# Kernel tuning notes

Hardware: AMD Instinct MI355X
Metric: run time of the kernel (lower is better)

Reference implementation:

```python
import jax, jax.numpy as jnp
import numpy as np

B = 8192
L = 2  # number of clipped photonic layers


def _pauli_z_matrix():
    # Z expectation per wire for each of the 16 basis states; wire 0 = MSB.
    k = np.arange(16)
    Z = np.stack([1 - 2 * ((k >> 3) & 1),
                  1 - 2 * ((k >> 2) & 1),
                  1 - 2 * ((k >> 1) & 1),
                  1 - 2 * (k & 1)], axis=1).astype(np.float32)
    return jnp.asarray(Z)  # (16, 4)


def setup_inputs() -> dict:
    key = jax.random.key(0)
    ks = jax.random.split(key, 14)
    x = jax.random.normal(ks[0], (B, 1, 28, 28), dtype=jnp.float32)
    # input photonic layer (no clip)
    w_in = 0.5 * jax.random.normal(ks[1], (2, 2), dtype=jnp.float32)
    b_in = 0.1 * jax.random.normal(ks[2], (2,), dtype=jnp.float32)
    scale_in = 1.0 + 0.1 * jax.random.normal(ks[3], (2,), dtype=jnp.float32)
    shift_in = 0.05 * jax.random.normal(ks[4], (2,), dtype=jnp.float32)
    # L clipped photonic layers (clip applied at construction in torch)
    Wc = jnp.clip(0.5 * jax.random.normal(ks[5], (L, 2, 2), dtype=jnp.float32), -5.0, 5.0)
    bc = jnp.clip(0.1 * jax.random.normal(ks[6], (L, 2), dtype=jnp.float32), -5.0, 5.0)
    scalec = 1.0 + 0.1 * jax.random.normal(ks[7], (L, 2), dtype=jnp.float32)
    shiftc = 0.05 * jax.random.normal(ks[8], (L, 2), dtype=jnp.float32)
    # final linear of classical branch: Linear(2, 1)
    w_out = 0.5 * jax.random.normal(ks[9], (1, 2), dtype=jnp.float32)
    b_out = 0.1 * jax.random.normal(ks[10], (1,), dtype=jnp.float32)
    # fixed random 16x16 unitary standing in for tq.RandomLayer(n_ops=8, 4 wires)
    rng = np.random.default_rng(0)
    A = rng.normal(size=(16, 16)) + 1j * rng.normal(size=(16, 16))
    Q, _ = np.linalg.qr(A)
    U_re = jnp.asarray(Q.real.astype(np.float32))
    U_im = jnp.asarray(Q.imag.astype(np.float32))
    # classifier Linear(785, 1)  (original declares 786 but combined feat is 785)
    w_cls = 0.03 * jax.random.normal(ks[11], (1, 785), dtype=jnp.float32)
    b_cls = 0.1 * jax.random.normal(ks[12], (1,), dtype=jnp.float32)
    return {"x": x, "w_in": w_in, "b_in": b_in, "scale_in": scale_in,
            "shift_in": shift_in, "Wc": Wc, "bc": bc, "scalec": scalec,
            "shiftc": shiftc, "w_out": w_out, "b_out": b_out,
            "U_re": U_re, "U_im": U_im, "w_cls": w_cls, "b_cls": b_cls}


def reference(x, w_in, b_in, scale_in, shift_in, Wc, bc, scalec, shiftc,
              w_out, b_out, U_re, U_im, w_cls, b_cls):
    bsz = x.shape[0]
    # ---- classical branch: mean/std features through photonic-style MLP ----
    mean = jnp.mean(x, axis=(1, 2, 3))[:, None]
    std = jnp.std(x, axis=(1, 2, 3), ddof=1)[:, None]  # torch unbiased std
    h = jnp.concatenate([mean, std], axis=1)  # (B, 2)
    h = jnp.tanh(h @ w_in.T + b_in) * scale_in + shift_in
    for i in range(Wc.shape[0]):
        h = jnp.tanh(h @ Wc[i].T + bc[i]) * scalec[i] + shiftc[i]
    cls_out = h @ w_out.T + b_out  # (B, 1)
    # ---- quantum branch: all 196 2x2 patches batched in one pass ----
    img = x.reshape(bsz, 28, 28)
    # (B,14,2,14,2) -> (B,14,14,2,2) -> (B,196,4) with patch pixel order
    # [x[r,c], x[r,c+1], x[r+1,c], x[r+1,c+1]] matching the torch loop.
    p = img.reshape(bsz, 14, 2, 14, 2).transpose(0, 1, 3, 2, 4).reshape(bsz, 196, 4)
    half = 0.5 * p
    a = jnp.stack([jnp.cos(half), jnp.sin(half)], axis=-1)  # (B,196,4,2) RY|0> amps
    # product state over 4 qubits -> (B,196,16)
    psi = jnp.einsum('bpi,bpj,bpk,bpl->bpijkl',
                     a[:, :, 0], a[:, :, 1], a[:, :, 2], a[:, :, 3]
                     ).reshape(bsz, 196, 16)
    re = psi @ U_re.T
    im = psi @ U_im.T
    probs = re * re + im * im  # (B,196,16)
    Z = _pauli_z_matrix()
    qfeat = (probs @ Z).reshape(bsz, 196 * 4)  # (B, 784)
    # ---- fuse + classify ----
    combined = jnp.concatenate([cls_out, qfeat], axis=1)  # (B, 785)
    logits = combined @ w_cls.T + b_cls
    return jax.nn.sigmoid(logits)
```

## Files before the change

### kernel.cpp

```cpp
#include <hip/hip_runtime.h>
#include <math.h>


#define NPIX 784
#define NPATCH 196

__global__ __launch_bounds__(256) void fraud_kernel(
    const float* __restrict__ x,
    const float* __restrict__ w_in,
    const float* __restrict__ b_in,
    const float* __restrict__ scale_in,
    const float* __restrict__ shift_in,
    const float* __restrict__ Wc,
    const float* __restrict__ bc,
    const float* __restrict__ scalec,
    const float* __restrict__ shiftc,
    const float* __restrict__ w_out,
    const float* __restrict__ b_out,
    const float* __restrict__ U_re,
    const float* __restrict__ U_im,
    const float* __restrict__ w_cls,
    const float* __restrict__ b_cls,
    float* __restrict__ out)
{
    const int img  = blockIdx.x;
    const int tid  = threadIdx.x;
    const int lane = tid & 63;
    const int wave = tid >> 6;

    const float* xp = x + (size_t)img * NPIX;

    float sum = 0.f, sumsq = 0.f, qsum = 0.f;

    if (tid < NPATCH) {
        const int r = tid / 14;
        const int c = tid - r * 14;
        const float2 top = *(const float2*)(xp + (2 * r) * 28 + 2 * c);
        const float2 bot = *(const float2*)(xp + (2 * r + 1) * 28 + 2 * c);
        const float x0 = top.x, x1 = top.y, x2 = bot.x, x3 = bot.y;

        sum   = x0 + x1 + x2 + x3;
        sumsq = x0 * x0 + x1 * x1 + x2 * x2 + x3 * x3;

        const float c0 = __cosf(0.5f * x0), s0 = __sinf(0.5f * x0);
        const float c1 = __cosf(0.5f * x1), s1 = __sinf(0.5f * x1);
        const float c2 = __cosf(0.5f * x2), s2 = __sinf(0.5f * x2);
        const float c3 = __cosf(0.5f * x3), s3 = __sinf(0.5f * x3);

        float p01[4] = { c0 * c1, c0 * s1, s0 * c1, s0 * s1 };
        float p23[4] = { c2 * c3, c2 * s3, s2 * c3, s2 * s3 };
        float psi[16];
        #pragma unroll
        for (int h = 0; h < 4; ++h) {
            #pragma unroll
            for (int l = 0; l < 4; ++l) {
                psi[h * 4 + l] = p01[h] * p23[l];
            }
        }

        const float wq0 = w_cls[1 + tid * 4 + 0];
        const float wq1 = w_cls[1 + tid * 4 + 1];
        const float wq2 = w_cls[1 + tid * 4 + 2];
        const float wq3 = w_cls[1 + tid * 4 + 3];
        float hi[4] = { wq0 + wq1, wq0 - wq1, -wq0 + wq1, -wq0 - wq1 };
        float lo[4] = { wq2 + wq3, wq2 - wq3, -wq2 + wq3, -wq2 - wq3 };

        #pragma unroll
        for (int k = 0; k < 16; ++k) {
            const float* ur = U_re + k * 16;
            const float* ui = U_im + k * 16;
            float re = 0.f, im = 0.f;
            #pragma unroll
            for (int m = 0; m < 16; ++m) {
                re = fmaf(ur[m], psi[m], re);
                im = fmaf(ui[m], psi[m], im);
            }
            const float prob = re * re + im * im;
            qsum = fmaf(prob, hi[k >> 2] + lo[k & 3], qsum);
        }
    }

    #pragma unroll
    for (int off = 32; off > 0; off >>= 1) {
        sum   += __shfl_down(sum,   off, 64);
        sumsq += __shfl_down(sumsq, off, 64);
        qsum  += __shfl_down(qsum,  off, 64);
    }

    __shared__ float red[3][4];
    if (lane == 0) {
        red[0][wave] = sum;
        red[1][wave] = sumsq;
        red[2][wave] = qsum;
    }
    __syncthreads();

    if (tid == 0) {
        const float S  = red[0][0] + red[0][1] + red[0][2] + red[0][3];
        const float SS = red[1][0] + red[1][1] + red[1][2] + red[1][3];
        const float QS = red[2][0] + red[2][1] + red[2][2] + red[2][3];

        const float mean = S * (1.f / 784.f);
        float var = (SS - S * S * (1.f / 784.f)) * (1.f / 783.f);
        var = fmaxf(var, 0.f);
        const float stdv = sqrtf(var);

        float h0 = mean, h1 = stdv;
        {
            const float t0 = tanhf(h0 * w_in[0] + h1 * w_in[1] + b_in[0]);
            const float t1 = tanhf(h0 * w_in[2] + h1 * w_in[3] + b_in[1]);
            h0 = t0 * scale_in[0] + shift_in[0];
            h1 = t1 * scale_in[1] + shift_in[1];
        }
        #pragma unroll
        for (int i = 0; i < 2; ++i) {
            const float t0 = tanhf(h0 * Wc[i * 4 + 0] + h1 * Wc[i * 4 + 1] + bc[i * 2 + 0]);
            const float t1 = tanhf(h0 * Wc[i * 4 + 2] + h1 * Wc[i * 4 + 3] + bc[i * 2 + 1]);
            h0 = t0 * scalec[i * 2 + 0] + shiftc[i * 2 + 0];
            h1 = t1 * scalec[i * 2 + 1] + shiftc[i * 2 + 1];
        }
        const float cls   = h0 * w_out[0] + h1 * w_out[1] + b_out[0];
        const float logit = b_cls[0] + w_cls[0] * cls + QS;
        out[img] = 1.f / (1.f + __expf(-logit));
    }
}

extern "C" void kernel_launch(void* const* d_in, const int* in_sizes, int n_in,
                              void* d_out, int out_size, void* d_ws, size_t ws_size,
                              hipStream_t stream) {
    const float* x        = (const float*)d_in[0];
    const float* w_in     = (const float*)d_in[1];
    const float* b_in     = (const float*)d_in[2];
    const float* scale_in = (const float*)d_in[3];
    const float* shift_in = (const float*)d_in[4];
    const float* Wc       = (const float*)d_in[5];
    const float* bc       = (const float*)d_in[6];
    const float* scalec   = (const float*)d_in[7];
    const float* shiftc   = (const float*)d_in[8];
    const float* w_out    = (const float*)d_in[9];
    const float* b_out    = (const float*)d_in[10];
    const float* U_re     = (const float*)d_in[11];
    const float* U_im     = (const float*)d_in[12];
    const float* w_cls    = (const float*)d_in[13];
    const float* b_cls    = (const float*)d_in[14];
    float* out = (float*)d_out;

    const int B = out_size;
    fraud_kernel<<<B, 256, 0, stream>>>(x, w_in, b_in, scale_in, shift_in,
                                        Wc, bc, scalec, shiftc, w_out, b_out,
                                        U_re, U_im, w_cls, b_cls, out);
}
```

Baseline: 119.4 us.

## Flatten patch work across batch with wave-split atomic reduction and finalize kernel

Replaces the one-block-per-image kernel (which left 60 of 256 threads idle) with a flat grid over all image patches. Each wave reduces its partial sums separately for up to two images and atomically adds them into a workspace. A second small kernel then computes the per-image statistics, the classical branch and the sigmoid. This adds a memset, an extra kernel launch and global atomics in exchange for full lane utilisation.

```diff
diff --git a/kernel.cpp b/kernel.cpp
--- a/kernel.cpp
+++ b/kernel.cpp
@@ -2,11 +2,99 @@
 #include <math.h>
 
 
-#define NPIX 784
 #define NPATCH 196
+#define NIMG   8192
+#define NTOTAL (NIMG * NPATCH)
 
-__global__ __launch_bounds__(256) void fraud_kernel(
+__global__ __launch_bounds__(256) void patch_kernel(
     const float* __restrict__ x,
+    const float* __restrict__ U_re,
+    const float* __restrict__ U_im,
+    const float* __restrict__ w_cls,
+    float* __restrict__ accS,
+    float* __restrict__ accSS,
+    float* __restrict__ accQ)
+{
+    const int g    = blockIdx.x * 256 + threadIdx.x;
+    const int img  = g / NPATCH;
+    const int p    = g - img * NPATCH;
+    const int r    = p / 14;
+    const int c    = p - r * 14;
+    const int lane = threadIdx.x & 63;
+
+    const float* xp = x + (size_t)img * 784;
+    const float2 top = *(const float2*)(xp + (2 * r) * 28 + 2 * c);
+    const float2 bot = *(const float2*)(xp + (2 * r + 1) * 28 + 2 * c);
+    const float x0 = top.x, x1 = top.y, x2 = bot.x, x3 = bot.y;
+
+    float sum   = x0 + x1 + x2 + x3;
+    float sumsq = x0 * x0 + x1 * x1 + x2 * x2 + x3 * x3;
+
+    const float c0 = __cosf(0.5f * x0), s0 = __sinf(0.5f * x0);
+    const float c1 = __cosf(0.5f * x1), s1 = __sinf(0.5f * x1);
+    const float c2 = __cosf(0.5f * x2), s2 = __sinf(0.5f * x2);
+    const float c3 = __cosf(0.5f * x3), s3 = __sinf(0.5f * x3);
+
+    float p01[4] = { c0 * c1, c0 * s1, s0 * c1, s0 * s1 };
+    float p23[4] = { c2 * c3, c2 * s3, s2 * c3, s2 * s3 };
+    float psi[16];
+    #pragma unroll
+    for (int h = 0; h < 4; ++h)
+        #pragma unroll
+        for (int l = 0; l < 4; ++l)
+            psi[h * 4 + l] = p01[h] * p23[l];
+
+    const float wq0 = w_cls[1 + p * 4 + 0];
+    const float wq1 = w_cls[1 + p * 4 + 1];
+    const float wq2 = w_cls[1 + p * 4 + 2];
+    const float wq3 = w_cls[1 + p * 4 + 3];
+    float hi[4] = { wq0 + wq1, wq0 - wq1, -wq0 + wq1, -wq0 - wq1 };
+    float lo[4] = { wq2 + wq3, wq2 - wq3, -wq2 + wq3, -wq2 - wq3 };
+
+    float qsum = 0.f;
+    #pragma unroll
+    for (int k = 0; k < 16; ++k) {
+        const float* ur = U_re + k * 16;
+        const float* ui = U_im + k * 16;
+        float re = 0.f, im = 0.f;
+        #pragma unroll
+        for (int m = 0; m < 16; ++m) {
+            re = fmaf(ur[m], psi[m], re);
+            im = fmaf(ui[m], psi[m], im);
+        }
+        const float prob = re * re + im * im;
+        qsum = fmaf(prob, hi[k >> 2] + lo[k & 3], qsum);
+    }
+
+    const int imgF = __builtin_amdgcn_readfirstlane(img);
+    const bool first = (img == imgF);
+    float aS = first ? sum   : 0.f;  float bS = sum   - aS;
+    float aV = first ? sumsq : 0.f;  float bV = sumsq - aV;
+    float aQ = first ? qsum  : 0.f;  float bQ = qsum  - aQ;
+
+    #pragma unroll
+    for (int off = 1; off < 64; off <<= 1) {
+        aS += __shfl_xor(aS, off, 64);  bS += __shfl_xor(bS, off, 64);
+        aV += __shfl_xor(aV, off, 64);  bV += __shfl_xor(bV, off, 64);
+        aQ += __shfl_xor(aQ, off, 64);  bQ += __shfl_xor(bQ, off, 64);
+    }
+
+    if (lane == 0) {
+        atomicAdd(accS  + imgF, aS);
+        atomicAdd(accSS + imgF, aV);
+        atomicAdd(accQ  + imgF, aQ);
+    }
+    if (lane == 63 && img != imgF) {
+        atomicAdd(accS  + img, bS);
+        atomicAdd(accSS + img, bV);
+        atomicAdd(accQ  + img, bQ);
+    }
+}
+
+__global__ __launch_bounds__(256) void final_kernel(
+    const float* __restrict__ accS,
+    const float* __restrict__ accSS,
+    const float* __restrict__ accQ,
     const float* __restrict__ w_in,
     const float* __restrict__ b_in,
     const float* __restrict__ scale_in,
@@ -17,112 +105,37 @@
     const float* __restrict__ shiftc,
     const float* __restrict__ w_out,
     const float* __restrict__ b_out,
-    const float* __restrict__ U_re,
-    const float* __restrict__ U_im,
     const float* __restrict__ w_cls,
     const float* __restrict__ b_cls,
     float* __restrict__ out)
 {
-    const int img  = blockIdx.x;
-    const int tid  = threadIdx.x;
-    const int lane = tid & 63;
-    const int wave = tid >> 6;
+    const int i = blockIdx.x * 256 + threadIdx.x;
+    const float S  = accS[i];
+    const float SS = accSS[i];
+    const float QS = accQ[i];
 
-    const float* xp = x + (size_t)img * NPIX;
+    const float mean = S * (1.f / 784.f);
+    float var = (SS - S * S * (1.f / 784.f)) * (1.f / 783.f);
+    var = fmaxf(var, 0.f);
+    const float stdv = sqrtf(var);
 
-    float sum = 0.f, sumsq = 0.f, qsum = 0.f;
-
-    if (tid < NPATCH) {
-        const int r = tid / 14;
-        const int c = tid - r * 14;
-        const float2 top = *(const float2*)(xp + (2 * r) * 28 + 2 * c);
-        const float2 bot = *(const float2*)(xp + (2 * r + 1) * 28 + 2 * c);
-        const float x0 = top.x, x1 = top.y, x2 = bot.x, x3 = bot.y;
-
-        sum   = x0 + x1 + x2 + x3;
-        sumsq = x0 * x0 + x1 * x1 + x2 * x2 + x3 * x3;
-
-        const float c0 = __cosf(0.5f * x0), s0 = __sinf(0.5f * x0);
-        const float c1 = __cosf(0.5f * x1), s1 = __sinf(0.5f * x1);
-        const float c2 = __cosf(0.5f * x2), s2 = __sinf(0.5f * x2);
-        const float c3 = __cosf(0.5f * x3), s3 = __sinf(0.5f * x3);
-
-        float p01[4] = { c0 * c1, c0 * s1, s0 * c1, s0 * s1 };
-        float p23[4] = { c2 * c3, c2 * s3, s2 * c3, s2 * s3 };
-        float psi[16];
-        #pragma unroll
-        for (int h = 0; h < 4; ++h) {
-            #pragma unroll
-            for (int l = 0; l < 4; ++l) {
-                psi[h * 4 + l] = p01[h] * p23[l];
-            }
-        }
-
-        const float wq0 = w_cls[1 + tid * 4 + 0];
-        const float wq1 = w_cls[1 + tid * 4 + 1];
-        const float wq2 = w_cls[1 + tid * 4 + 2];
-        const float wq3 = w_cls[1 + tid * 4 + 3];
-        float hi[4] = { wq0 + wq1, wq0 - wq1, -wq0 + wq1, -wq0 - wq1 };
-        float lo[4] = { wq2 + wq3, wq2 - wq3, -wq2 + wq3, -wq2 - wq3 };
-
-        #pragma unroll
-        for (int k = 0; k < 16; ++k) {
-            const float* ur = U_re + k * 16;
-            const float* ui = U_im + k * 16;
-            float re = 0.f, im = 0.f;
-            #pragma unroll
-            for (int m = 0; m < 16; ++m) {
-                re = fmaf(ur[m], psi[m], re);
-                im = fmaf(ui[m], psi[m], im);
-            }
-            const float prob = re * re + im * im;
-            qsum = fmaf(prob, hi[k >> 2] + lo[k & 3], qsum);
-        }
+    float h0 = mean, h1 = stdv;
+    {
+        const float t0 = tanhf(h0 * w_in[0] + h1 * w_in[1] + b_in[0]);
+        const float t1 = tanhf(h0 * w_in[2] + h1 * w_in[3] + b_in[1]);
+        h0 = t0 * scale_in[0] + shift_in[0];
+        h1 = t1 * scale_in[1] + shift_in[1];
     }
-
     #pragma unroll
-    for (int off = 32; off > 0; off >>= 1) {
-        sum   += __shfl_down(sum,   off, 64);
-        sumsq += __shfl_down(sumsq, off, 64);
-        qsum  += __shfl_down(qsum,  off, 64);
+    for (int l = 0; l < 2; ++l) {
+        const float t0 = tanhf(h0 * Wc[l * 4 + 0] + h1 * Wc[l * 4 + 1] + bc[l * 2 + 0]);
+        const float t1 = tanhf(h0 * Wc[l * 4 + 2] + h1 * Wc[l * 4 + 3] + bc[l * 2 + 1]);
+        h0 = t0 * scalec[l * 2 + 0] + shiftc[l * 2 + 0];
+        h1 = t1 * scalec[l * 2 + 1] + shiftc[l * 2 + 1];
     }
-
-    __shared__ float red[3][4];
-    if (lane == 0) {
-        red[0][wave] = sum;
-        red[1][wave] = sumsq;
-        red[2][wave] = qsum;
-    }
-    __syncthreads();
-
-    if (tid == 0) {
-        const float S  = red[0][0] + red[0][1] + red[0][2] + red[0][3];
-        const float SS = red[1][0] + red[1][1] + red[1][2] + red[1][3];
-        const float QS = red[2][0] + red[2][1] + red[2][2] + red[2][3];
-
-        const float mean = S * (1.f / 784.f);
-        float var = (SS - S * S * (1.f / 784.f)) * (1.f / 783.f);
-        var = fmaxf(var, 0.f);
-        const float stdv = sqrtf(var);
-
-        float h0 = mean, h1 = stdv;
-        {
-            const float t0 = tanhf(h0 * w_in[0] + h1 * w_in[1] + b_in[0]);
-            const float t1 = tanhf(h0 * w_in[2] + h1 * w_in[3] + b_in[1]);
-            h0 = t0 * scale_in[0] + shift_in[0];
-            h1 = t1 * scale_in[1] + shift_in[1];
-        }
-        #pragma unroll
-        for (int i = 0; i < 2; ++i) {
-            const float t0 = tanhf(h0 * Wc[i * 4 + 0] + h1 * Wc[i * 4 + 1] + bc[i * 2 + 0]);
-            const float t1 = tanhf(h0 * Wc[i * 4 + 2] + h1 * Wc[i * 4 + 3] + bc[i * 2 + 1]);
-            h0 = t0 * scalec[i * 2 + 0] + shiftc[i * 2 + 0];
-            h1 = t1 * scalec[i * 2 + 1] + shiftc[i * 2 + 1];
-        }
-        const float cls   = h0 * w_out[0] + h1 * w_out[1] + b_out[0];
-        const float logit = b_cls[0] + w_cls[0] * cls + QS;
-        out[img] = 1.f / (1.f + __expf(-logit));
-    }
+    const float cls   = h0 * w_out[0] + h1 * w_out[1] + b_out[0];
+    const float logit = b_cls[0] + w_cls[0] * cls + QS;
+    out[i] = 1.f / (1.f + __expf(-logit));
 }
 
 extern "C" void kernel_launch(void* const* d_in, const int* in_sizes, int n_in,
@@ -145,8 +158,16 @@
     const float* b_cls    = (const float*)d_in[14];
     float* out = (float*)d_out;
 
-    const int B = out_size;
-    fraud_kernel<<<B, 256, 0, stream>>>(x, w_in, b_in, scale_in, shift_in,
-                                        Wc, bc, scalec, shiftc, w_out, b_out,
-                                        U_re, U_im, w_cls, b_cls, out);
+    float* accS  = (float*)d_ws;
+    float* accSS = accS + NIMG;
+    float* accQ  = accSS + NIMG;
+
+    hipMemsetAsync(d_ws, 0, 3 * NIMG * sizeof(float), stream);
+
+    patch_kernel<<<NTOTAL / 256, 256, 0, stream>>>(x, U_re, U_im, w_cls,
+                                                   accS, accSS, accQ);
+    final_kernel<<<NIMG / 256, 256, 0, stream>>>(accS, accSS, accQ,
+                                                 w_in, b_in, scale_in, shift_in,
+                                                 Wc, bc, scalec, shiftc,
+                                                 w_out, b_out, w_cls, b_cls, out);
 }
```

After: 127.4 us. 1.07x slower.

## Compute patch unitary products with bf16 MFMA instead of scalar FMAs

Applied to the files above, without the earlier changes.

Each thread's 16-amplitude product state is packed to bf16 and staged in LDS. Waves then compute the complex unitary product with 16x16x32 bf16 MFMA instructions, with U held in register fragments and the classifier weights cached in LDS. This replaces 512 scalar FMAs per patch with a few matrix instructions per 16 patches, at the cost of bf16 rounding of amplitudes and U, extra LDS traffic and a barrier. The grid size is also hardcoded to 8192 images instead of using the output size.

```diff
diff --git a/kernel.cpp b/kernel.cpp
--- a/kernel.cpp
+++ b/kernel.cpp
@@ -1,9 +1,24 @@
 #include <hip/hip_runtime.h>
+#include <hip/hip_bf16.h>
 #include <math.h>
 
 
-#define NPIX 784
 #define NPATCH 196
+#define NIMG   8192
+#define ROWB   80
+
+typedef __bf16 bf16x8 __attribute__((ext_vector_type(8)));
+typedef float  f32x4  __attribute__((ext_vector_type(4)));
+
+union Frag { bf16x8 v; uint4 u; unsigned us[4]; };
+
+static __device__ inline unsigned short bfbits(float f) {
+    __hip_bfloat16 h = __float2bfloat16(f);
+    unsigned short s; __builtin_memcpy(&s, &h, 2); return s;
+}
+static __device__ inline unsigned packbf(float lo, float hi) {
+    return (unsigned)bfbits(lo) | ((unsigned)bfbits(hi) << 16);
+}
 
 __global__ __launch_bounds__(256) void fraud_kernel(
     const float* __restrict__ x,
@@ -23,75 +38,112 @@
     const float* __restrict__ b_cls,
     float* __restrict__ out)
 {
-    const int img  = blockIdx.x;
+    __shared__ __align__(16) unsigned char lds[256 * ROWB];
+    __shared__ __align__(16) float wlds[784];
+    __shared__ float red[3][4];
+
     const int tid  = threadIdx.x;
     const int lane = tid & 63;
-    const int wave = tid >> 6;
-
-    const float* xp = x + (size_t)img * NPIX;
-
-    float sum = 0.f, sumsq = 0.f, qsum = 0.f;
-
+    const int wv   = tid >> 6;
+    const int n16  = lane & 15;
+    const int q    = lane >> 4;
+    const int img  = blockIdx.x;
+
+    for (int i = tid; i < 784; i += 256) wlds[i] = w_cls[1 + i];
+
+    Frag bre, bim;
+    bre.u = make_uint4(0u, 0u, 0u, 0u);
+    bim.u = make_uint4(0u, 0u, 0u, 0u);
+    if (q < 2) {
+        const float* pr = U_re + n16 * 16 + q * 8;
+        const float* pi = U_im + n16 * 16 + q * 8;
+        bre.us[0] = packbf(pr[0], pr[1]); bre.us[1] = packbf(pr[2], pr[3]);
+        bre.us[2] = packbf(pr[4], pr[5]); bre.us[3] = packbf(pr[6], pr[7]);
+        bim.us[0] = packbf(pi[0], pi[1]); bim.us[1] = packbf(pi[2], pi[3]);
+        bim.us[2] = packbf(pi[4], pi[5]); bim.us[3] = packbf(pi[6], pi[7]);
+    }
+
+    const float* xp = x + (size_t)img * 784;
+    float sum = 0.f, sumsq = 0.f;
+    uint4 lo = make_uint4(0u, 0u, 0u, 0u);
+    uint4 hi = make_uint4(0u, 0u, 0u, 0u);
     if (tid < NPATCH) {
-        const int r = tid / 14;
-        const int c = tid - r * 14;
-        const float2 top = *(const float2*)(xp + (2 * r) * 28 + 2 * c);
-        const float2 bot = *(const float2*)(xp + (2 * r + 1) * 28 + 2 * c);
+        const int rr = tid / 14;
+        const int cc = tid - rr * 14;
+        const float2 top = *(const float2*)(xp + (2 * rr) * 28 + 2 * cc);
+        const float2 bot = *(const float2*)(xp + (2 * rr + 1) * 28 + 2 * cc);
         const float x0 = top.x, x1 = top.y, x2 = bot.x, x3 = bot.y;
 
         sum   = x0 + x1 + x2 + x3;
         sumsq = x0 * x0 + x1 * x1 + x2 * x2 + x3 * x3;
 
-        const float c0 = __cosf(0.5f * x0), s0 = __sinf(0.5f * x0);
-        const float c1 = __cosf(0.5f * x1), s1 = __sinf(0.5f * x1);
-        const float c2 = __cosf(0.5f * x2), s2 = __sinf(0.5f * x2);
-        const float c3 = __cosf(0.5f * x3), s3 = __sinf(0.5f * x3);
-
-        float p01[4] = { c0 * c1, c0 * s1, s0 * c1, s0 * s1 };
-        float p23[4] = { c2 * c3, c2 * s3, s2 * c3, s2 * s3 };
-        float psi[16];
+        float s0, c0, s1, c1, s2, c2, s3, c3;
+        __sincosf(0.5f * x0, &s0, &c0);
+        __sincosf(0.5f * x1, &s1, &c1);
+        __sincosf(0.5f * x2, &s2, &c2);
+        __sincosf(0.5f * x3, &s3, &c3);
+
+        const float a01[4] = { c0 * c1, c0 * s1, s0 * c1, s0 * s1 };
+        const float a23[4] = { c2 * c3, c2 * s3, s2 * c3, s2 * s3 };
+
+        lo.x = packbf(a01[0] * a23[0], a01[0] * a23[1]);
+        lo.y = packbf(a01[0] * a23[2], a01[0] * a23[3]);
+        lo.z = packbf(a01[1] * a23[0], a01[1] * a23[1]);
+        lo.w = packbf(a01[1] * a23[2], a01[1] * a23[3]);
+        hi.x = packbf(a01[2] * a23[0], a01[2] * a23[1]);
+        hi.y = packbf(a01[2] * a23[2], a01[2] * a23[3]);
+        hi.z = packbf(a01[3] * a23[0], a01[3] * a23[1]);
+        hi.w = packbf(a01[3] * a23[2], a01[3] * a23[3]);
+    }
+    unsigned* row = (unsigned*)(lds + tid * ROWB);
+    *(uint4*)(row)      = lo;
+    *(uint4*)(row + 4)  = hi;
+    *(uint4*)(row + 8)  = make_uint4(0u, 0u, 0u, 0u);
+    *(uint4*)(row + 12) = make_uint4(0u, 0u, 0u, 0u);
+    __syncthreads();
+
+    const float sg0 = (n16 & 8) ? -1.f : 1.f;
+    const float sg1 = (n16 & 4) ? -1.f : 1.f;
+    const float sg2 = (n16 & 2) ? -1.f : 1.f;
+    const float sg3 = (n16 & 1) ? -1.f : 1.f;
+
+    float qacc = 0.f;
+    const unsigned char* wb = lds + wv * 64 * ROWB;
+
+    auto do_tile = [&](int t) {
+        Frag a;
+        a.u = *(const uint4*)(wb + (t * 16 + n16) * ROWB + q * 16);
+        f32x4 cr = {0.f, 0.f, 0.f, 0.f}, ci = {0.f, 0.f, 0.f, 0.f};
+        cr = __builtin_amdgcn_mfma_f32_16x16x32_bf16(a.v, bre.v, cr, 0, 0, 0);
+        ci = __builtin_amdgcn_mfma_f32_16x16x32_bf16(a.v, bim.v, ci, 0, 0, 0);
         #pragma unroll
-        for (int h = 0; h < 4; ++h) {
-            #pragma unroll
-            for (int l = 0; l < 4; ++l) {
-                psi[h * 4 + l] = p01[h] * p23[l];
+        for (int j = 0; j < 4; ++j) {
+            const int m = wv * 64 + t * 16 + q * 4 + j;
+            float zc = 0.f;
+            if (m < NPATCH) {
+                const float4 wq = *(const float4*)(wlds + 4 * m);
+                zc = wq.x * sg0 + wq.y * sg1 + wq.z * sg2 + wq.w * sg3;
             }
+            const float prob = cr[j] * cr[j] + ci[j] * ci[j];
+            qacc = fmaf(prob, zc, qacc);
         }
-
-        const float wq0 = w_cls[1 + tid * 4 + 0];
-        const float wq1 = w_cls[1 + tid * 4 + 1];
-        const float wq2 = w_cls[1 + tid * 4 + 2];
-        const float wq3 = w_cls[1 + tid * 4 + 3];
-        float hi[4] = { wq0 + wq1, wq0 - wq1, -wq0 + wq1, -wq0 - wq1 };
-        float lo[4] = { wq2 + wq3, wq2 - wq3, -wq2 + wq3, -wq2 - wq3 };
-
-        #pragma unroll
-        for (int k = 0; k < 16; ++k) {
-            const float* ur = U_re + k * 16;
-            const float* ui = U_im + k * 16;
-            float re = 0.f, im = 0.f;
-            #pragma unroll
-            for (int m = 0; m < 16; ++m) {
-                re = fmaf(ur[m], psi[m], re);
-                im = fmaf(ui[m], psi[m], im);
-            }
-            const float prob = re * re + im * im;
-            qsum = fmaf(prob, hi[k >> 2] + lo[k & 3], qsum);
-        }
+    };
+    if (wv < 3) {
+        do_tile(0); do_tile(1); do_tile(2); do_tile(3);
+    } else {
+        do_tile(0);
     }
 
     #pragma unroll
-    for (int off = 32; off > 0; off >>= 1) {
-        sum   += __shfl_down(sum,   off, 64);
-        sumsq += __shfl_down(sumsq, off, 64);
-        qsum  += __shfl_down(qsum,  off, 64);
-    }
-
-    __shared__ float red[3][4];
+    for (int off = 1; off < 64; off <<= 1) {
+        sum   += __shfl_xor(sum,   off, 64);
+        sumsq += __shfl_xor(sumsq, off, 64);
+        qacc  += __shfl_xor(qacc,  off, 64);
+    }
     if (lane == 0) {
-        red[0][wave] = sum;
-        red[1][wave] = sumsq;
-        red[2][wave] = qsum;
+        red[0][wv] = sum;
+        red[1][wv] = sumsq;
+        red[2][wv] = qacc;
     }
     __syncthreads();
 
@@ -113,11 +165,11 @@
             h1 = t1 * scale_in[1] + shift_in[1];
         }
         #pragma unroll
-        for (int i = 0; i < 2; ++i) {
-            const float t0 = tanhf(h0 * Wc[i * 4 + 0] + h1 * Wc[i * 4 + 1] + bc[i * 2 + 0]);
-            const float t1 = tanhf(h0 * Wc[i * 4 + 2] + h1 * Wc[i * 4 + 3] + bc[i * 2 + 1]);
-            h0 = t0 * scalec[i * 2 + 0] + shiftc[i * 2 + 0];
-            h1 = t1 * scalec[i * 2 + 1] + shiftc[i * 2 + 1];
+        for (int l = 0; l < 2; ++l) {
+            const float t0 = tanhf(h0 * Wc[l * 4 + 0] + h1 * Wc[l * 4 + 1] + bc[l * 2 + 0]);
+            const float t1 = tanhf(h0 * Wc[l * 4 + 2] + h1 * Wc[l * 4 + 3] + bc[l * 2 + 1]);
+            h0 = t0 * scalec[l * 2 + 0] + shiftc[l * 2 + 0];
+            h1 = t1 * scalec[l * 2 + 1] + shiftc[l * 2 + 1];
         }
         const float cls   = h0 * w_out[0] + h1 * w_out[1] + b_out[0];
         const float logit = b_cls[0] + w_cls[0] * cls + QS;
@@ -145,8 +197,7 @@
     const float* b_cls    = (const float*)d_in[14];
     float* out = (float*)d_out;
 
-    const int B = out_size;
-    fraud_kernel<<<B, 256, 0, stream>>>(x, w_in, b_in, scale_in, shift_in,
-                                        Wc, bc, scalec, shiftc, w_out, b_out,
-                                        U_re, U_im, w_cls, b_cls, out);
-}
+    fraud_kernel<<<NIMG, 256, 0, stream>>>(x, w_in, b_in, scale_in, shift_in,
+                                           Wc, bc, scalec, shiftc, w_out, b_out,
+                                           U_re, U_im, w_cls, b_cls, out);
+}
```

New measurement: 115.7 us. 1.03x faster.
